# Kernel tuning notes

Hardware: AMD Instinct MI355X
Metric: run time of the kernel (lower is better)

The kernel has to match this reference:

```python
import jax, jax.numpy as jnp
import numpy as np

B, LC, LS, D = 16384, 100, 12, 10  # C:(B,LC,D), x1:(B,LS,D)


def setup_inputs() -> dict:
    key = jax.random.key(0)
    ks = jax.random.split(key, 7)
    u = lambda k, shp: jax.random.uniform(k, shp, jnp.float32, -0.05, 0.05)  # keras 'uniform' init
    return {
        "C": jax.random.normal(ks[0], (B, LC, D), jnp.float32),
        "x1": jax.random.normal(ks[1], (B, LS, D), jnp.float32),
        "W": u(ks[2], (D, D)),      # kernelW (10,10)
        "Ws": u(ks[3], (LS, LS)),   # kernelWs (12,12)
        "Wc": u(ks[4], (LC, LC)),   # kernelWc (100,100)
        "Was": u(ks[5], (D, 1)),    # kernelas (10,1)
        "Wac": u(ks[6], (D, 1)),    # kernelac (10,1)
    }


def reference(C, x1, W, Ws, Wc, Was, Wac):
    # C: (B,100,10), x1: (B,12,10)
    RNN = jnp.swapaxes(x1, 1, 2)                      # (B,10,12)
    f = jnp.einsum('bld,de->ble', C, W)               # (B,100,10)
    F = jnp.tanh(jnp.matmul(f, RNN))                  # (B,100,12)
    s = jnp.einsum('bdl,lm->bdm', RNN, Ws)            # (B,10,12)
    c = jnp.einsum('bdl,lm->bdm', jnp.swapaxes(C, 1, 2), Wc)  # (B,10,100)
    Hs = jnp.tanh(s + jnp.matmul(c, F))               # (B,10,12)
    Hc = jnp.tanh(c + jnp.matmul(s, jnp.swapaxes(F, 1, 2)))   # (B,10,100)
    # softmax over the last (size-1) axis, exactly as K.softmax does here
    As = jax.nn.softmax(jnp.einsum('bdl,do->blo', Hs, Was), axis=-1)  # (B,12,1)
    Ac = jax.nn.softmax(jnp.einsum('bdl,do->blo', Hc, Wac), axis=-1)  # (B,100,1)
    As = jnp.swapaxes(As, 1, 2)                       # (B,1,12)
    Ac = jnp.swapaxes(Ac, 1, 2)                       # (B,1,100)
    sfinal = jnp.matmul(As, jnp.swapaxes(RNN, 1, 2))  # (B,1,10)
    cfinal = jnp.matmul(Ac, C)                        # (B,1,10)
    return jnp.concatenate([sfinal, cfinal], axis=-1) # (B,1,20)
```

## Files before the change

### kernel.cpp

```cpp
#include <hip/hip_runtime.h>
#include <hip/hip_bf16.h>


#define BATCHES 16384

__global__ __launch_bounds__(64) void coattention_sum_kernel(
    const float* __restrict__ C,
    const float* __restrict__ x1,
    float* __restrict__ out)
{
    const int lane = threadIdx.x;
    const int half = lane >> 5;
    const int u = blockIdx.x * 32 + (lane & 31);
    const int b = u / 5;
    const int p = u - b * 5;

    const float2* __restrict__ cp =
        reinterpret_cast<const float2*>(C) + (size_t)b * 500 + half * 250 + p;
    const float2* __restrict__ xp =
        reinterpret_cast<const float2*>(x1) + (size_t)b * 60 + half * 30 + p;

    float sx = 0.f, sy = 0.f;
#pragma unroll
    for (int l = 0; l < 6; ++l) { float2 v = xp[l * 5]; sx += v.x; sy += v.y; }

    float cx = 0.f, cy = 0.f;
#pragma unroll
    for (int l = 0; l < 50; ++l) { float2 v = cp[l * 5]; cx += v.x; cy += v.y; }

    sx += __shfl_xor(sx, 32); sy += __shfl_xor(sy, 32);
    cx += __shfl_xor(cx, 32); cy += __shfl_xor(cy, 32);

    if (half == 0) {
        float2* o = reinterpret_cast<float2*>(out) + (size_t)b * 10;
        o[p]     = make_float2(sx, sy);
        o[5 + p] = make_float2(cx, cy);
    }
}

extern "C" void kernel_launch(void* const* d_in, const int* in_sizes, int n_in,
                              void* d_out, int out_size, void* d_ws, size_t ws_size,
                              hipStream_t stream) {
    const float* C  = (const float*)d_in[0];
    const float* x1 = (const float*)d_in[1];
    float* out = (float*)d_out;

    const int units = BATCHES * 5;
    const int grid = units / 32;
    coattention_sum_kernel<<<grid, 64, 0, stream>>>(C, x1, out);
}
```

Measured before the change: 18.35 us.

## Use float4 loads with ten threads per batch and LDS atomic reduction

Remaps work so each 320-thread block handles 32 batches, with ten threads per batch reading strided float4 chunks of C and x1. This replaces the earlier float2 loads and cross-half shuffle. Because each float4 chunk's lane positions repeat every 10 elements, each thread always feeds the same four output columns. Per-thread partial sums are combined through shared-memory atomics, and the result is written as coalesced float2 stores. The aim is wider memory transactions and fewer load instructions, at the cost of LDS atomics and two block barriers.

```diff
diff --git a/kernel.cpp b/kernel.cpp
--- a/kernel.cpp
+++ b/kernel.cpp
@@ -4,48 +4,64 @@
 
 #define BATCHES 16384
 
-__global__ __launch_bounds__(64) void coattention_sum_kernel(
-    const float* __restrict__ C,
-    const float* __restrict__ x1,
-    float* __restrict__ out)
+__global__ __launch_bounds__(320) void coattention_sum_kernel(
+    const float4* __restrict__ C4,
+    const float4* __restrict__ x14,
+    float2* __restrict__ out2)
 {
-    const int lane = threadIdx.x;
-    const int half = lane >> 5;
-    const int u = blockIdx.x * 32 + (lane & 31);
-    const int b = u / 5;
-    const int p = u - b * 5;
+    __shared__ __align__(16) float sums[32 * 20];
 
-    const float2* __restrict__ cp =
-        reinterpret_cast<const float2*>(C) + (size_t)b * 500 + half * 250 + p;
-    const float2* __restrict__ xp =
-        reinterpret_cast<const float2*>(x1) + (size_t)b * 60 + half * 30 + p;
+    const int t = threadIdx.x;
+    sums[t] = 0.f;
+    sums[t + 320] = 0.f;
+    __syncthreads();
 
-    float sx = 0.f, sy = 0.f;
+    const int bl = t / 10;
+    const int j  = t - bl * 10;
+    const int b  = blockIdx.x * 32 + bl;
+
+    const float4* __restrict__ cp = C4 + (size_t)b * 250 + j;
+    const float4* __restrict__ xp = x14 + (size_t)b * 30 + j;
+
+    float c0 = 0.f, c1 = 0.f, c2 = 0.f, c3 = 0.f;
 #pragma unroll
-    for (int l = 0; l < 6; ++l) { float2 v = xp[l * 5]; sx += v.x; sy += v.y; }
+    for (int g = 0; g < 25; ++g) {
+        float4 v = cp[g * 10];
+        c0 += v.x; c1 += v.y; c2 += v.z; c3 += v.w;
+    }
 
-    float cx = 0.f, cy = 0.f;
+    float s0 = 0.f, s1 = 0.f, s2 = 0.f, s3 = 0.f;
 #pragma unroll
-    for (int l = 0; l < 50; ++l) { float2 v = cp[l * 5]; cx += v.x; cy += v.y; }
+    for (int g = 0; g < 3; ++g) {
+        float4 v = xp[g * 10];
+        s0 += v.x; s1 += v.y; s2 += v.z; s3 += v.w;
+    }
 
-    sx += __shfl_xor(sx, 32); sy += __shfl_xor(sy, 32);
-    cx += __shfl_xor(cx, 32); cy += __shfl_xor(cy, 32);
+    const int base = 4 * j;
+    const int k0 = base % 10, k1 = (base + 1) % 10;
+    const int k2 = (base + 2) % 10, k3 = (base + 3) % 10;
 
-    if (half == 0) {
-        float2* o = reinterpret_cast<float2*>(out) + (size_t)b * 10;
-        o[p]     = make_float2(sx, sy);
-        o[5 + p] = make_float2(cx, cy);
-    }
+    float* row = &sums[bl * 20];
+    atomicAdd(&row[k0], s0);
+    atomicAdd(&row[k1], s1);
+    atomicAdd(&row[k2], s2);
+    atomicAdd(&row[k3], s3);
+    atomicAdd(&row[10 + k0], c0);
+    atomicAdd(&row[10 + k1], c1);
+    atomicAdd(&row[10 + k2], c2);
+    atomicAdd(&row[10 + k3], c3);
+    __syncthreads();
+
+    out2[(size_t)blockIdx.x * 320 + t] = make_float2(sums[2 * t], sums[2 * t + 1]);
 }
 
 extern "C" void kernel_launch(void* const* d_in, const int* in_sizes, int n_in,
                               void* d_out, int out_size, void* d_ws, size_t ws_size,
                               hipStream_t stream) {
-    const float* C  = (const float*)d_in[0];
-    const float* x1 = (const float*)d_in[1];
-    float* out = (float*)d_out;
+    const float4* C4  = (const float4*)d_in[0];
+    const float4* x14 = (const float4*)d_in[1];
+    float2* out2 = (float2*)d_out;
 
-    const int units = BATCHES * 5;
-    const int grid = units / 32;
-    coattention_sum_kernel<<<grid, 64, 0, stream>>>(C, x1, out);
+    const int grid = BATCHES / 32;
+    coattention_sum_kernel<<<grid, 320, 0, stream>>>(C4, x14, out2);
 }
```

After: 19.50 us. +6.3%, slower.
